# Performance work log

Hardware: AMD Instinct MI355X
Metric: run time of the kernel (lower is better)

The kernel has to match this reference:

```python
import jax, jax.numpy as jnp
import numpy as np

B, S, D, H, RANK, NC = 2, 2048, 1024, 16, 128, 16
DH = D // H


def setup_inputs() -> dict:
    key = jax.random.key(0)
    ks = jax.random.split(key, 10)
    x = jax.random.normal(ks[0], (B, S, D), jnp.float32)
    # causal mask, broadcast over batch and heads like torch's [B,1,S,S]
    mask = jnp.tril(jnp.ones((S, S), dtype=bool))[None, None]
    # orthogonal-ish init approximated by scaled gaussian
    compress_neurons = jax.random.normal(ks[1], (NC, D, RANK), jnp.float32) / np.sqrt(D)
    router_Q = jax.random.normal(ks[2], (NC, D), jnp.float32) * 0.02
    router_K = jax.random.normal(ks[3], (NC, D), jnp.float32) * 0.02
    router_V = jax.random.normal(ks[4], (NC, D), jnp.float32) * 0.02
    wQ = jax.random.normal(ks[5], (D, RANK), jnp.float32) / np.sqrt(RANK)
    wK = jax.random.normal(ks[6], (D, RANK), jnp.float32) / np.sqrt(RANK)
    wV = jax.random.normal(ks[7], (D, RANK), jnp.float32) / np.sqrt(RANK)
    wO = jax.random.normal(ks[8], (D, D), jnp.float32) / np.sqrt(D)
    return {"x": x, "mask": mask, "compress_neurons": compress_neurons,
            "router_Q": router_Q, "router_K": router_K, "router_V": router_V,
            "wQ": wQ, "wK": wK, "wV": wV, "wO": wO}


def reference(x, mask, compress_neurons, router_Q, router_K, router_V, wQ, wK, wV, wO):
    def compress(router_w):
        # router scores -> softmax over all n_compress neurons
        w = jax.nn.softmax(jnp.einsum('bsd,nd->bsn', x, router_w), axis=-1)  # [B,S,NC]
        # softmax-weighted sum of all neuron projections (fused einsum)
        return jnp.einsum('bsd,ndr,bsn->bsr', x, compress_neurons, w)  # [B,S,RANK]

    hQ = compress(router_Q)
    hK = compress(router_K)
    hV = compress(router_V)
    # expand rank -> d_model (Linear weight [D,RANK]), then split heads
    Q = jnp.einsum('bsr,dr->bsd', hQ, wQ).reshape(B, S, H, DH).transpose(0, 2, 1, 3)
    K = jnp.einsum('bsr,dr->bsd', hK, wK).reshape(B, S, H, DH).transpose(0, 2, 1, 3)
    V = jnp.einsum('bsr,dr->bsd', hV, wV).reshape(B, S, H, DH).transpose(0, 2, 1, 3)
    scores = jnp.einsum('bhqd,bhkd->bhqk', Q, K) / np.sqrt(DH)  # [B,H,S,S]
    scores = jnp.where(mask, scores, -jnp.inf)
    attn = jax.nn.softmax(scores, axis=-1)
    attn_out = jnp.einsum('bhqk,bhkd->bhqd', attn, V)
    attn_out = attn_out.transpose(0, 2, 1, 3).reshape(B, S, D)
    # dropout omitted (eval mode / dropout=0)
    return jnp.einsum('bsd,ed->bse', attn_out, wO)
```

## Files before the change

### kernel.cpp

```cpp
#include <hip/hip_runtime.h>
#include <hip/hip_bf16.h>
#include <math.h>

#define B_ 2
#define S_ 2048
#define D_ 1024
#define H_ 16
#define RANK_ 128
#define NC_ 16
#define DH_ 64
#define T_ (B_*S_)
#define NZ_ 2176

typedef __attribute__((ext_vector_type(8))) __bf16 bf16x8;
typedef __attribute__((ext_vector_type(8))) unsigned short u16x8;
typedef __attribute__((ext_vector_type(4))) float f32x4;

#if __has_builtin(__builtin_amdgcn_exp2f)
#define EXP2F(x) __builtin_amdgcn_exp2f(x)
#else
#define EXP2F(x) exp2f(x)
#endif

__device__ __forceinline__ unsigned short f2bu(float f) {
    __hip_bfloat16 h = __float2bfloat16(f);
    unsigned short u; __builtin_memcpy(&u, &h, 2); return u;
}
__device__ __forceinline__ float bu2f(unsigned short u) {
    __hip_bfloat16 h; __builtin_memcpy(&h, &u, 2); return __bfloat162float(h);
}

__device__ __forceinline__ void gl_lds16(const unsigned short* g, unsigned short* l) {
    __builtin_amdgcn_global_load_lds(
        (const __attribute__((address_space(1))) void*)g,
        (__attribute__((address_space(3))) void*)l, 16, 0, 0);
}

__device__ __forceinline__ bool sniff_f32(const unsigned* __restrict__ p) {
    int votes = 0;
    #pragma unroll
    for (int i = 0; i < 64; i++) {
        unsigned e = (p[i] >> 23) & 0xFFu;
        votes += (e >= 0x60u && e <= 0x8Fu) ? 1 : 0;
    }
    return votes >= 32;
}

struct Cvt { const void* src[9]; unsigned short* dst[9]; const void* C; unsigned short* Ct; };

__global__ __launch_bounds__(256) void k_inputs(Cvt cv,
    const unsigned* __restrict__ probe)
{
    bool f32 = sniff_f32(probe);
    if (blockIdx.x < 512) {
        int bid = blockIdx.x;
        int d0 = (bid & 15) * 64, r0 = ((bid >> 4) & 1) * 64, n = bid >> 5;
        __shared__ unsigned short tile[64][65];
        for (int idx = threadIdx.x; idx < 4096; idx += 256) {
            int row = idx >> 6, col = idx & 63;
            size_t si = ((size_t)n*D_ + d0 + row)*RANK_ + r0 + col;
            tile[row][col] = f32 ? f2bu(((const float*)cv.C)[si])
                                 : ((const unsigned short*)cv.C)[si];
        }
        __syncthreads();
        for (int idx = threadIdx.x; idx < 4096; idx += 256) {
            int row = idx >> 6, col = idx & 63;
            cv.Ct[((size_t)(n*RANK_ + r0 + row))*D_ + d0 + col] = tile[col][row];
        }
        return;
    }
    const int offs[9] = {0, 4194304, 4210688, 4227072, 4243456,
                         4259840, 4390912, 4521984, 4653056};
    const int total = 5701632;
    int nconv = gridDim.x - 512;
    int stride = nconv * 256;
    for (int i = (blockIdx.x - 512) * 256 + threadIdx.x; i < total; i += stride) {
        int seg = 0;
        #pragma unroll
        for (int s = 1; s < 9; s++) seg += (i >= offs[s]) ? 1 : 0;
        int local = i - offs[seg];
        const void* sp = cv.src[seg];
        unsigned short v = 0;
        if (sp) v = f32 ? f2bu(((const float*)sp)[local]) : ((const unsigned short*)sp)[local];
        cv.dst[seg][local] = v;
    }
}

template<int MT, int MODE>
__global__ __launch_bounds__(256) void k_mfma_gemm(const unsigned short* __restrict__ A,
    const unsigned short* __restrict__ Bm, void* __restrict__ Cout,
    const unsigned* __restrict__ probe, int M, int N, int K)
{
    bool f32out = false;
    if (MODE == 2) f32out = sniff_f32(probe);
    __shared__ __align__(16) unsigned short As[MT*32*32];
    __shared__ __align__(16) unsigned short Bs[128*32];
    const int tid = threadIdx.x;
    const int wv = tid >> 6, lane = tid & 63;
    const int wm = (wv >> 1) * (MT*16), wn = (wv & 1) * 64;
    const int quad = lane >> 4, l16 = lane & 15;
    const int m0 = blockIdx.x * (MT*32), n0 = blockIdx.y * 128;

    const f32x4 z4 = {0.f, 0.f, 0.f, 0.f};
    f32x4 acc[MT][4];
    #pragma unroll
    for (int i = 0; i < MT; i++)
        #pragma unroll
        for (int j = 0; j < 4; j++) acc[i][j] = z4;

    for (int k0 = 0; k0 < K; k0 += 32) {
        __syncthreads();
        #pragma unroll
        for (int c = 0; c < MT/2; c++) {
            int idx = wv*64 + c*256 + lane;
            gl_lds16(A + (size_t)(m0 + (idx >> 2))*K + k0 + (idx & 3)*8,
                     &As[(wv*64 + c*256)*8]);
        }
        #pragma unroll
        for (int c = 0; c < 2; c++) {
            int idx = wv*64 + c*256 + lane;
            gl_lds16(Bm + (size_t)(n0 + (idx >> 2))*K + k0 + (idx & 3)*8,
                     &Bs[(wv*64 + c*256)*8]);
        }
        __syncthreads();
        bf16x8 af[MT], bfr[4];
        #pragma unroll
        for (int mt = 0; mt < MT; mt++) af[mt]  = *(const bf16x8*)&As[(wm + mt*16 + l16)*32 + quad*8];
        #pragma unroll
        for (int nt = 0; nt < 4; nt++) bfr[nt] = *(const bf16x8*)&Bs[(wn + nt*16 + l16)*32 + quad*8];
        #pragma unroll
        for (int mt = 0; mt < MT; mt++)
            #pragma unroll
            for (int nt = 0; nt < 4; nt++)
                acc[mt][nt] = __builtin_amdgcn_mfma_f32_16x16x32_bf16(af[mt], bfr[nt], acc[mt][nt], 0, 0, 0);
    }
    #pragma unroll
    for (int mt = 0; mt < MT; mt++)
        #pragma unroll
        for (int nt = 0; nt < 4; nt++) {
            int col = n0 + wn + nt*16 + l16;
            #pragma unroll
            for (int r = 0; r < 4; r++) {
                int rowg = m0 + wm + mt*16 + quad*4 + r;
                float v = acc[mt][nt][r];
                if (MODE == 2 && f32out) ((float*)Cout)[(size_t)rowg*N + col] = v;
                else  ((unsigned short*)Cout)[(size_t)rowg*N + col] = f2bu(v);
            }
        }
}

__global__ __launch_bounds__(256) void k_qkv2(const unsigned short* __restrict__ h3,
    const unsigned short* __restrict__ wqkv, unsigned short* __restrict__ QKb,
    unsigned short* __restrict__ Vtg)
{
    __shared__ __align__(16) unsigned short As[128*32];
    __shared__ __align__(16) unsigned short Bs[128*32];
    const int tid = threadIdx.x;
    const int wv = tid >> 6, lane = tid & 63;
    const int wm = (wv >> 1) * 64, wn = (wv & 1) * 64;
    const int quad = lane >> 4, l16 = lane & 15;

    const bool vt = (blockIdx.x >= 512);
    int m0, n0;
    const unsigned short *A, *Bm;
    float scale = 1.f;
    if (!vt) {
        int id = blockIdx.x;
        m0 = (id & 31) * 128;
        n0 = (id >> 5) * 128;
        int w = n0 >> 10;
        A  = h3 + (size_t)w * T_ * RANK_ + (size_t)m0 * RANK_;
        Bm = wqkv + (size_t)w * D_ * RANK_ + (size_t)(n0 & 1023) * RANK_;
        if (w == 0) scale = 0.125f * 1.44269504f;
    } else {
        int id = blockIdx.x - 512;
        m0 = (id & 7) * 128;
        n0 = (id >> 3) * 128;
        A  = wqkv + (size_t)2 * D_ * RANK_ + (size_t)m0 * RANK_;
        Bm = h3 + (size_t)2 * T_ * RANK_ + (size_t)n0 * RANK_;
    }

    const f32x4 z4 = {0.f, 0.f, 0.f, 0.f};
    f32x4 acc[4][4];
    #pragma unroll
    for (int i = 0; i < 4; i++)
        #pragma unroll
        for (int j = 0; j < 4; j++) acc[i][j] = z4;

    for (int k0 = 0; k0 < RANK_; k0 += 32) {
        __syncthreads();
        #pragma unroll
        for (int c = 0; c < 2; c++) {
            int idx = wv*64 + c*256 + lane;
            gl_lds16(A  + (size_t)(idx >> 2)*RANK_ + k0 + (idx & 3)*8,
                     &As[(wv*64 + c*256)*8]);
            gl_lds16(Bm + (size_t)(idx >> 2)*RANK_ + k0 + (idx & 3)*8,
                     &Bs[(wv*64 + c*256)*8]);
        }
        __syncthreads();
        bf16x8 af[4], bfr[4];
        #pragma unroll
        for (int mt = 0; mt < 4; mt++) af[mt]  = *(const bf16x8*)&As[(wm + mt*16 + l16)*32 + quad*8];
        #pragma unroll
        for (int nt = 0; nt < 4; nt++) bfr[nt] = *(const bf16x8*)&Bs[(wn + nt*16 + l16)*32 + quad*8];
        #pragma unroll
        for (int mt = 0; mt < 4; mt++)
            #pragma unroll
            for (int nt = 0; nt < 4; nt++)
                acc[mt][nt] = __builtin_amdgcn_mfma_f32_16x16x32_bf16(af[mt], bfr[nt], acc[mt][nt], 0, 0, 0);
    }
    #pragma unroll
    for (int mt = 0; mt < 4; mt++)
        #pragma unroll
        for (int nt = 0; nt < 4; nt++) {
            #pragma unroll
            for (int r = 0; r < 4; r++) {
                int rowg = m0 + wm + mt*16 + quad*4 + r;
                int col  = n0 + wn + nt*16 + l16;
                float v = acc[mt][nt][r] * scale;
                if (!vt) {
                    QKb[(size_t)(col >> 10)*T_*D_ + (size_t)rowg*D_ + (col & 1023)]
                        = f2bu(v);
                } else {
                    size_t vrow = (size_t)((col >> 11)*H_ + (rowg >> 6))*64 + (rowg & 63);
                    Vtg[vrow*S_ + (col & 2047)] = f2bu(v);
                }
            }
        }
}

__global__ __launch_bounds__(256) void k_hreduce(const unsigned short* __restrict__ z,
    unsigned short* __restrict__ h)
{
    int t0 = blockIdx.x * 2;
    int tg = threadIdx.x >> 7, r = threadIdx.x & 127;
    int t = t0 + tg;
    __shared__ float sc[2][48];
    __shared__ float wl[2][3][16];
    if (threadIdx.x < 96) {
        int tk = threadIdx.x / 48, j = threadIdx.x % 48;
        sc[tk][j] = bu2f(z[(size_t)(t0 + tk)*NZ_ + 2048 + j]);
    }
    __syncthreads();
    if (threadIdx.x < 6) {
        int tk = threadIdx.x / 3, w = threadIdx.x % 3;
        float m = -INFINITY;
        for (int n = 0; n < 16; n++) m = fmaxf(m, sc[tk][w*16 + n]);
        float s = 0.f, e[16];
        for (int n = 0; n < 16; n++) { e[n] = __expf(sc[tk][w*16 + n] - m); s += e[n]; }
        float inv = 1.f / s;
        for (int n = 0; n < 16; n++) wl[tk][w][n] = e[n] * inv;
    }
    __syncthreads();
    const unsigned short* zr = z + (size_t)t * NZ_;
    float acc[3] = {0.f, 0.f, 0.f};
    #pragma unroll
    for (int n = 0; n < NC_; n++) {
        float zv = bu2f(zr[n*RANK_ + r]);
        #pragma unroll
        for (int w = 0; w < 3; w++) acc[w] += wl[tg][w][n] * zv;
    }
    #pragma unroll
    for (int w = 0; w < 3; w++) h[((size_t)w*T_ + t)*RANK_ + r] = f2bu(acc[w]);
}

__global__ __launch_bounds__(256) void k_flash_mfma(const unsigned short* __restrict__ Qm,
    const unsigned short* __restrict__ Km, const unsigned short* __restrict__ Vtg,
    unsigned short* __restrict__ Om)
{
    const int p = blockIdx.x, hh = blockIdx.y, b = blockIdx.z;
    __shared__ __align__(16) unsigned short Ks[2][128*64];
    __shared__ __align__(16) unsigned short Vs[2][64*128];
    __shared__ __align__(16) unsigned short Ps[64*128];
    const int tid = threadIdx.x;
    const int w = tid >> 6, lane = tid & 63;
    const int quad = lane >> 4, l16 = lane & 15;
    const size_t base  = ((size_t)b * S_) * D_ + (size_t)hh * DH_;
    const size_t vbase = (size_t)((b*H_ + hh) * 64) * S_;
    const f32x4 z4 = {0.f, 0.f, 0.f, 0.f};

    for (int rep = 0; rep < 2; rep++) {
        const int qt = rep ? (31 - p) : p;

        bf16x8 aq[2];
        #pragma unroll
        for (int s = 0; s < 2; s++)
            aq[s] = *(const bf16x8*)(Qm + base + (size_t)(qt*64 + w*16 + l16)*D_ + s*32 + quad*8);

        f32x4 oacc[4];
        #pragma unroll
        for (int nt = 0; nt < 4; nt++) oacc[nt] = z4;
        float lsum[4] = {0.f, 0.f, 0.f, 0.f};

        const int nkt = (qt >> 1) + 1;

        __syncthreads();
        #pragma unroll
        for (int c = 0; c < 4; c++) {
            int idx = c*256 + tid;
            int row = idx >> 3, j = (idx & 7) ^ (row & 7);
            gl_lds16(Km + base + (size_t)row*D_ + j*8, &Ks[0][(c*256 + (w<<6))*8]);
        }
        #pragma unroll
        for (int c = 0; c < 4; c++) {
            int idx = c*256 + tid;
            int row = idx >> 4, j = (idx & 15) ^ (row & 7);
            gl_lds16(Vtg + vbase + (size_t)row*S_ + j*8, &Vs[0][(c*256 + (w<<6))*8]);
        }

        for (int kt = 0; kt < nkt; kt++) {
            const int cur = kt & 1;
            __syncthreads();

            if (kt + 1 < nkt) {
                #pragma unroll
                for (int c = 0; c < 4; c++) {
                    int idx = c*256 + tid;
                    int row = idx >> 3, j = (idx & 7) ^ (row & 7);
                    gl_lds16(Km + base + (size_t)((kt+1)*128 + row)*D_ + j*8,
                             &Ks[1-cur][(c*256 + (w<<6))*8]);
                }
                #pragma unroll
                for (int c = 0; c < 4; c++) {
                    int idx = c*256 + tid;
                    int row = idx >> 4, j = (idx & 15) ^ (row & 7);
                    gl_lds16(Vtg + vbase + (size_t)row*S_ + (kt+1)*128 + j*8,
                             &Vs[1-cur][(c*256 + (w<<6))*8]);
                }
            }

            f32x4 sacc[8];
            #pragma unroll
            for (int nt = 0; nt < 8; nt++) sacc[nt] = z4;
            #pragma unroll
            for (int s = 0; s < 2; s++)
                #pragma unroll
                for (int nt = 0; nt < 8; nt++) {
                    int row = nt*16 + l16;
                    int cc = (s*4 + quad) ^ (row & 7);
                    bf16x8 bk = *(const bf16x8*)&Ks[cur][row*64 + cc*8];
                    sacc[nt] = __builtin_amdgcn_mfma_f32_16x16x32_bf16(aq[s], bk, sacc[nt], 0, 0, 0);
                }
            if (kt == (qt >> 1)) {
                #pragma unroll
                for (int nt = 0; nt < 8; nt++) {
                    int key = kt*128 + nt*16 + l16;
                    #pragma unroll
                    for (int r = 0; r < 4; r++)
                        if (key > qt*64 + w*16 + quad*4 + r) sacc[nt][r] = -INFINITY;
                }
            }
            #pragma unroll
            for (int r = 0; r < 4; r++) {
                float rs = 0.f;
                int tokl = quad*4 + r;
                #pragma unroll
                for (int nt = 0; nt < 8; nt++) {
                    float pv = EXP2F(sacc[nt][r]);
                    rs += pv;
                    int pc = (nt*2 + (l16 >> 3)) ^ (tokl & 7);
                    Ps[(w*16 + tokl)*128 + pc*8 + (l16 & 7)] = f2bu(pv);
                }
                lsum[r] += rs;
            }
            #pragma unroll
            for (int s = 0; s < 4; s++) {
                int pc = (s*4 + quad) ^ (l16 & 7);
                bf16x8 ap = *(const bf16x8*)&Ps[(w*16 + l16)*128 + pc*8];
                #pragma unroll
                for (int nt = 0; nt < 4; nt++) {
                    int row = nt*16 + l16;
                    int cc = (s*4 + quad) ^ (row & 7);
                    bf16x8 bv = *(const bf16x8*)&Vs[cur][row*128 + cc*8];
                    oacc[nt] = __builtin_amdgcn_mfma_f32_16x16x32_bf16(ap, bv, oacc[nt], 0, 0, 0);
                }
            }
        }
        #pragma unroll
        for (int r = 0; r < 4; r++) {
            float l = lsum[r];
            #pragma unroll
            for (int off = 1; off < 16; off <<= 1) l += __shfl_xor(l, off, 64);
            float inv = 1.f / l;
            int tok = qt*64 + w*16 + quad*4 + r;
            #pragma unroll
            for (int nt = 0; nt < 4; nt++)
                Om[base + (size_t)tok*D_ + nt*16 + l16] = f2bu(oacc[nt][r] * inv);
        }
    }
}

extern "C" void kernel_launch(void* const* d_in, const int* in_sizes, int n_in,
                              void* d_out, int out_size, void* d_ws, size_t ws_size,
                              hipStream_t stream)
{
    const unsigned* probe = (const unsigned*)d_in[0];

    unsigned short* u = (unsigned short*)d_ws;
    unsigned short* xc   = u;               size_t o = (size_t)T_*D_;
    unsigned short* wqkv = u + o;           o += (size_t)3*D_*RANK_;
    unsigned short* wOc  = u + o;           o += (size_t)D_*D_;
    unsigned short* Ct   = u + o;           o += (size_t)NZ_*D_;
    unsigned short* h3   = u + o;           o += (size_t)3*T_*RANK_;
    unsigned short* QKb  = u + o;           o += (size_t)2*T_*D_;
    unsigned short* Vtg  = u + o;           o += (size_t)T_*D_;
    unsigned short* z    = u + o;           o += (size_t)T_*NZ_;
    unsigned short* attnb= u + o;           o += (size_t)T_*D_;

    unsigned short* Rp = Ct + (size_t)2048*D_;
    unsigned short* Qb = QKb;
    unsigned short* Kb = QKb + (size_t)T_*D_;

    Cvt cv;
    cv.src[0] = d_in[0]; cv.dst[0] = xc;
    cv.src[1] = d_in[3]; cv.dst[1] = Rp;
    cv.src[2] = d_in[4]; cv.dst[2] = Rp + 16384;
    cv.src[3] = d_in[5]; cv.dst[3] = Rp + 32768;
    cv.src[4] = nullptr; cv.dst[4] = Rp + 49152;
    cv.src[5] = d_in[6]; cv.dst[5] = wqkv;
    cv.src[6] = d_in[7]; cv.dst[6] = wqkv + 131072;
    cv.src[7] = d_in[8]; cv.dst[7] = wqkv + 262144;
    cv.src[8] = d_in[9]; cv.dst[8] = wOc;
    cv.C = d_in[2]; cv.Ct = Ct;
    k_inputs<<<512 + 2048, 256, 0, stream>>>(cv, probe);

    k_mfma_gemm<4,0><<<dim3(T_/128, NZ_/128), 256, 0, stream>>>(
        xc, Ct, z, nullptr, T_, NZ_, D_);

    k_hreduce<<<T_/2, 256, 0, stream>>>(z, h3);

    k_qkv2<<<768, 256, 0, stream>>>(h3, wqkv, QKb, Vtg);

    k_flash_mfma<<<dim3(16, H_, B_), 256, 0, stream>>>(Qb, Kb, Vtg, attnb);

    k_mfma_gemm<2,2><<<dim3(T_/64, D_/128), 256, 0, stream>>>(
        attnb, wOc, d_out, probe, T_, D_, D_);
}
```

Baseline: 237.1 us.

## Process both paired query tiles in one pass over shared K/V tiles

The flash attention kernel used to handle its two query tiles (p and 31-p) one after the other, streaming K and V from global memory separately for each. Now it keeps both tiles' Q fragments and accumulators live and walks the longer key range once. Each K/V tile in LDS feeds both tiles, and the shorter tile drops out once its causal range ends. This cuts K/V global traffic and barrier count, at the cost of more registers per thread, which may lower occupancy.

```diff
diff --git a/kernel.cpp b/kernel.cpp
--- a/kernel.cpp
+++ b/kernel.cpp
@@ -279,56 +279,58 @@
     const size_t vbase = (size_t)((b*H_ + hh) * 64) * S_;
     const f32x4 z4 = {0.f, 0.f, 0.f, 0.f};
 
-    for (int rep = 0; rep < 2; rep++) {
-        const int qt = rep ? (31 - p) : p;
-
-        bf16x8 aq[2];
-        #pragma unroll
-        for (int s = 0; s < 2; s++)
-            aq[s] = *(const bf16x8*)(Qm + base + (size_t)(qt*64 + w*16 + l16)*D_ + s*32 + quad*8);
-
-        f32x4 oacc[4];
-        #pragma unroll
-        for (int nt = 0; nt < 4; nt++) oacc[nt] = z4;
-        float lsum[4] = {0.f, 0.f, 0.f, 0.f};
-
-        const int nkt = (qt >> 1) + 1;
-
-        __syncthreads();
-        #pragma unroll
-        for (int c = 0; c < 4; c++) {
-            int idx = c*256 + tid;
-            int row = idx >> 3, j = (idx & 7) ^ (row & 7);
-            gl_lds16(Km + base + (size_t)row*D_ + j*8, &Ks[0][(c*256 + (w<<6))*8]);
-        }
-        #pragma unroll
-        for (int c = 0; c < 4; c++) {
-            int idx = c*256 + tid;
-            int row = idx >> 4, j = (idx & 15) ^ (row & 7);
-            gl_lds16(Vtg + vbase + (size_t)row*S_ + j*8, &Vs[0][(c*256 + (w<<6))*8]);
-        }
-
-        for (int kt = 0; kt < nkt; kt++) {
-            const int cur = kt & 1;
-            __syncthreads();
-
-            if (kt + 1 < nkt) {
-                #pragma unroll
-                for (int c = 0; c < 4; c++) {
-                    int idx = c*256 + tid;
-                    int row = idx >> 3, j = (idx & 7) ^ (row & 7);
-                    gl_lds16(Km + base + (size_t)((kt+1)*128 + row)*D_ + j*8,
-                             &Ks[1-cur][(c*256 + (w<<6))*8]);
-                }
-                #pragma unroll
-                for (int c = 0; c < 4; c++) {
-                    int idx = c*256 + tid;
-                    int row = idx >> 4, j = (idx & 15) ^ (row & 7);
-                    gl_lds16(Vtg + vbase + (size_t)row*S_ + (kt+1)*128 + j*8,
-                             &Vs[1-cur][(c*256 + (w<<6))*8]);
-                }
-            }
-
+    const int qtA = p, qtB = 31 - p;
+    const int nktA = (qtA >> 1) + 1, nktB = (qtB >> 1) + 1;
+
+    bf16x8 aqA[2], aqB[2];
+    #pragma unroll
+    for (int s = 0; s < 2; s++) {
+        aqA[s] = *(const bf16x8*)(Qm + base + (size_t)(qtA*64 + w*16 + l16)*D_ + s*32 + quad*8);
+        aqB[s] = *(const bf16x8*)(Qm + base + (size_t)(qtB*64 + w*16 + l16)*D_ + s*32 + quad*8);
+    }
+
+    f32x4 oaccA[4], oaccB[4];
+    #pragma unroll
+    for (int nt = 0; nt < 4; nt++) { oaccA[nt] = z4; oaccB[nt] = z4; }
+    float lsumA[4] = {0.f,0.f,0.f,0.f}, lsumB[4] = {0.f,0.f,0.f,0.f};
+
+    #pragma unroll
+    for (int c = 0; c < 4; c++) {
+        int idx = c*256 + tid;
+        int row = idx >> 3, j = (idx & 7) ^ (row & 7);
+        gl_lds16(Km + base + (size_t)row*D_ + j*8, &Ks[0][(c*256 + (w<<6))*8]);
+    }
+    #pragma unroll
+    for (int c = 0; c < 4; c++) {
+        int idx = c*256 + tid;
+        int row = idx >> 4, j = (idx & 15) ^ (row & 7);
+        gl_lds16(Vtg + vbase + (size_t)row*S_ + j*8, &Vs[0][(c*256 + (w<<6))*8]);
+    }
+
+    for (int kt = 0; kt < nktB; kt++) {
+        const int cur = kt & 1;
+        __syncthreads();
+
+        if (kt + 1 < nktB) {
+            #pragma unroll
+            for (int c = 0; c < 4; c++) {
+                int idx = c*256 + tid;
+                int row = idx >> 3, j = (idx & 7) ^ (row & 7);
+                gl_lds16(Km + base + (size_t)((kt+1)*128 + row)*D_ + j*8,
+                         &Ks[1-cur][(c*256 + (w<<6))*8]);
+            }
+            #pragma unroll
+            for (int c = 0; c < 4; c++) {
+                int idx = c*256 + tid;
+                int row = idx >> 4, j = (idx & 15) ^ (row & 7);
+                gl_lds16(Vtg + vbase + (size_t)row*S_ + (kt+1)*128 + j*8,
+                         &Vs[1-cur][(c*256 + (w<<6))*8]);
+            }
+        }
+
+        const bool Aact = (kt < nktA);
+
+        {
             f32x4 sacc[8];
             #pragma unroll
             for (int nt = 0; nt < 8; nt++) sacc[nt] = z4;
@@ -339,15 +341,15 @@
                     int row = nt*16 + l16;
                     int cc = (s*4 + quad) ^ (row & 7);
                     bf16x8 bk = *(const bf16x8*)&Ks[cur][row*64 + cc*8];
-                    sacc[nt] = __builtin_amdgcn_mfma_f32_16x16x32_bf16(aq[s], bk, sacc[nt], 0, 0, 0);
-                }
-            if (kt == (qt >> 1)) {
+                    sacc[nt] = __builtin_amdgcn_mfma_f32_16x16x32_bf16(aqB[s], bk, sacc[nt], 0, 0, 0);
+                }
+            if (kt == nktB - 1) {
                 #pragma unroll
                 for (int nt = 0; nt < 8; nt++) {
                     int key = kt*128 + nt*16 + l16;
                     #pragma unroll
                     for (int r = 0; r < 4; r++)
-                        if (key > qt*64 + w*16 + quad*4 + r) sacc[nt][r] = -INFINITY;
+                        if (key > qtB*64 + w*16 + quad*4 + r) sacc[nt][r] = -INFINITY;
                 }
             }
             #pragma unroll
@@ -361,7 +363,7 @@
                     int pc = (nt*2 + (l16 >> 3)) ^ (tokl & 7);
                     Ps[(w*16 + tokl)*128 + pc*8 + (l16 & 7)] = f2bu(pv);
                 }
-                lsum[r] += rs;
+                lsumB[r] += rs;
             }
             #pragma unroll
             for (int s = 0; s < 4; s++) {
@@ -372,20 +374,74 @@
                     int row = nt*16 + l16;
                     int cc = (s*4 + quad) ^ (row & 7);
                     bf16x8 bv = *(const bf16x8*)&Vs[cur][row*128 + cc*8];
-                    oacc[nt] = __builtin_amdgcn_mfma_f32_16x16x32_bf16(ap, bv, oacc[nt], 0, 0, 0);
-                }
-            }
-        }
-        #pragma unroll
-        for (int r = 0; r < 4; r++) {
-            float l = lsum[r];
-            #pragma unroll
-            for (int off = 1; off < 16; off <<= 1) l += __shfl_xor(l, off, 64);
-            float inv = 1.f / l;
-            int tok = qt*64 + w*16 + quad*4 + r;
-            #pragma unroll
-            for (int nt = 0; nt < 4; nt++)
-                Om[base + (size_t)tok*D_ + nt*16 + l16] = f2bu(oacc[nt][r] * inv);
+                    oaccB[nt] = __builtin_amdgcn_mfma_f32_16x16x32_bf16(ap, bv, oaccB[nt], 0, 0, 0);
+                }
+            }
+        }
+        if (Aact) {
+            f32x4 sacc[8];
+            #pragma unroll
+            for (int nt = 0; nt < 8; nt++) sacc[nt] = z4;
+            #pragma unroll
+            for (int s = 0; s < 2; s++)
+                #pragma unroll
+                for (int nt = 0; nt < 8; nt++) {
+                    int row = nt*16 + l16;
+                    int cc = (s*4 + quad) ^ (row & 7);
+                    bf16x8 bk = *(const bf16x8*)&Ks[cur][row*64 + cc*8];
+                    sacc[nt] = __builtin_amdgcn_mfma_f32_16x16x32_bf16(aqA[s], bk, sacc[nt], 0, 0, 0);
+                }
+            if (kt == nktA - 1) {
+                #pragma unroll
+                for (int nt = 0; nt < 8; nt++) {
+                    int key = kt*128 + nt*16 + l16;
+                    #pragma unroll
+                    for (int r = 0; r < 4; r++)
+                        if (key > qtA*64 + w*16 + quad*4 + r) sacc[nt][r] = -INFINITY;
+                }
+            }
+            #pragma unroll
+            for (int r = 0; r < 4; r++) {
+                float rs = 0.f;
+                int tokl = quad*4 + r;
+                #pragma unroll
+                for (int nt = 0; nt < 8; nt++) {
+                    float pv = EXP2F(sacc[nt][r]);
+                    rs += pv;
+                    int pc = (nt*2 + (l16 >> 3)) ^ (tokl & 7);
+                    Ps[(w*16 + tokl)*128 + pc*8 + (l16 & 7)] = f2bu(pv);
+                }
+                lsumA[r] += rs;
+            }
+            #pragma unroll
+            for (int s = 0; s < 4; s++) {
+                int pc = (s*4 + quad) ^ (l16 & 7);
+                bf16x8 ap = *(const bf16x8*)&Ps[(w*16 + l16)*128 + pc*8];
+                #pragma unroll
+                for (int nt = 0; nt < 4; nt++) {
+                    int row = nt*16 + l16;
+                    int cc = (s*4 + quad) ^ (row & 7);
+                    bf16x8 bv = *(const bf16x8*)&Vs[cur][row*128 + cc*8];
+                    oaccA[nt] = __builtin_amdgcn_mfma_f32_16x16x32_bf16(ap, bv, oaccA[nt], 0, 0, 0);
+                }
+            }
+        }
+    }
+    #pragma unroll
+    for (int r = 0; r < 4; r++) {
+        float la = lsumA[r], lb = lsumB[r];
+        #pragma unroll
+        for (int off = 1; off < 16; off <<= 1) {
+            la += __shfl_xor(la, off, 64);
+            lb += __shfl_xor(lb, off, 64);
+        }
+        float invA = 1.f / la, invB = 1.f / lb;
+        int tokA = qtA*64 + w*16 + quad*4 + r;
+        int tokB = qtB*64 + w*16 + quad*4 + r;
+        #pragma unroll
+        for (int nt = 0; nt < 4; nt++) {
+            Om[base + (size_t)tokA*D_ + nt*16 + l16] = f2bu(oaccA[nt][r] * invA);
+            Om[base + (size_t)tokB*D_ + nt*16 + l16] = f2bu(oaccB[nt][r] * invB);
         }
     }
 }
```

Result: slower. 256.4 us (+8.2%).
